# Kernel optimization log

Measured on AMD Instinct MI355X. Metric: run time of the kernel, lower is better.

The kernel has to match this reference:

```python
import jax, jax.numpy as jnp
import numpy as np

# Static config (matches init_kwargs)
DIM, HEADS = 192, 6
PL, LAT, LON = 8, 96, 180
WP, WL, WW = 2, 6, 12          # window size (pressure, lat, lon)
SP, SL, SW = 1, 3, 6           # shift size
N = WP * WL * WW               # tokens per window = 144
NPL, NLAT, NLON = PL // WP, LAT // WL, LON // WW   # 4, 16, 15
NW = NPL * NLAT                # type_of_windows = 64 (lat/pl-dependent bias)
HD = DIM // HEADS              # 32
L = PL * LAT * LON
BIAS_LEN = (2 * WW - 1) * WL * WL * WP * WP   # 3312
EPS = 1e-5


def _position_index():
    # Earth-specific relative position index (Pangu): absolute-position
    # dependence along pressure and latitude, relative along longitude.
    zi = np.arange(WP); zj = -np.arange(WP) * WP
    hi = np.arange(WL); hj = -np.arange(WL) * WL
    w = np.arange(WW)
    c1 = np.stack(np.meshgrid(zi, hi, w, indexing='ij')).reshape(3, -1)
    c2 = np.stack(np.meshgrid(zj, hj, w, indexing='ij')).reshape(3, -1)
    c = (c1[:, :, None] - c2[:, None, :]).transpose(1, 2, 0).copy()
    c[:, :, 2] += WW - 1
    c[:, :, 1] *= 2 * WW - 1
    c[:, :, 0] *= (2 * WW - 1) * WL * WL
    return c.sum(-1)  # (N, N) in [0, BIAS_LEN)


def _attn_mask():
    # Shifted-window mask: lon is periodic on the globe (roll only), so
    # masking is applied along pressure and latitude boundaries only.
    img = np.zeros((1, PL, LAT, LON, 1), np.float32)
    cnt = 0
    for pl in (slice(0, -WP), slice(-WP, -SP), slice(-SP, None)):
        for la in (slice(0, -WL), slice(-WL, -SL), slice(-SL, None)):
            img[:, pl, la, :, :] = cnt
            cnt += 1
    mw = img.reshape(1, NPL, WP, NLAT, WL, NLON, WW, 1)
    mw = mw.transpose(0, 5, 1, 3, 2, 4, 6, 7).reshape(NLON, NW, N)
    am = mw[:, :, None, :] - mw[:, :, :, None]
    return np.where(am != 0, -100.0, 0.0).astype(np.float32)  # (NLON, NW, N, N)


POS_IDX = jnp.asarray(_position_index())
ATTN_MASK = jnp.asarray(_attn_mask())


def layer_norm(x, g, b):
    m = x.mean(-1, keepdims=True)
    v = ((x - m) ** 2).mean(-1, keepdims=True)
    return (x - m) * jax.lax.rsqrt(v + EPS) * g + b


def setup_inputs() -> dict:
    key = jax.random.key(0)
    ks = jax.random.split(key, 10)
    s = 0.02
    return {
        'x': jax.random.normal(ks[0], (1, L, DIM), jnp.float32),
        'norm1_g': jnp.ones((DIM,), jnp.float32),
        'norm1_b': jnp.zeros((DIM,), jnp.float32),
        'qkv_w': jax.random.normal(ks[1], (DIM, 3 * DIM), jnp.float32) * s,
        'qkv_b': jnp.zeros((3 * DIM,), jnp.float32),
        'earth_bias': jax.random.normal(ks[2], (BIAS_LEN, NW, HEADS), jnp.float32) * s,
        'proj_w': jax.random.normal(ks[3], (DIM, DIM), jnp.float32) * s,
        'proj_b': jnp.zeros((DIM,), jnp.float32),
        'norm2_g': jnp.ones((DIM,), jnp.float32),
        'norm2_b': jnp.zeros((DIM,), jnp.float32),
        'fc1_w': jax.random.normal(ks[4], (DIM, 4 * DIM), jnp.float32) * s,
        'fc1_b': jnp.zeros((4 * DIM,), jnp.float32),
        'fc2_w': jax.random.normal(ks[5], (4 * DIM, DIM), jnp.float32) * s,
        'fc2_b': jnp.zeros((DIM,), jnp.float32),
    }


def reference(x, norm1_g, norm1_b, qkv_w, qkv_b, earth_bias, proj_w, proj_b,
              norm2_g, norm2_b, fc1_w, fc1_b, fc2_w, fc2_b):
    B, Ltok, C = x.shape
    shortcut = x
    h = layer_norm(x, norm1_g, norm1_b).reshape(B, PL, LAT, LON, C)
    # shifted windows (lon is periodic -> plain roll)
    h = jnp.roll(h, shift=(-SP, -SL, -SW), axis=(1, 2, 3))
    # window partition -> (B*NLON, NW, N, C); lon windows folded into batch
    xw = h.reshape(B, NPL, WP, NLAT, WL, NLON, WW, C)
    xw = xw.transpose(0, 5, 1, 3, 2, 4, 6, 7).reshape(B * NLON, NW, N, C)
    # earth-specific attention
    qkv = (xw @ qkv_w + qkv_b).reshape(B * NLON, NW, N, 3, HEADS, HD)
    qkv = qkv.transpose(3, 0, 1, 4, 2, 5)  # (3, B_, NW, H, N, HD)
    q, k, v = qkv[0], qkv[1], qkv[2]
    attn = jnp.einsum('bwhnd,bwhmd->bwhnm', q * (HD ** -0.5), k)
    bias = earth_bias[POS_IDX].reshape(N, N, NW, HEADS).transpose(2, 3, 0, 1)
    attn = attn + bias[None]                        # (B_, NW, H, N, N)
    attn = attn.reshape(B, NLON, NW, HEADS, N, N) + ATTN_MASK[None, :, :, None]
    attn = jax.nn.softmax(attn.reshape(B * NLON, NW, HEADS, N, N), axis=-1)
    out = jnp.einsum('bwhnm,bwhmd->bwhnd', attn, v)
    out = out.transpose(0, 1, 3, 2, 4).reshape(B * NLON, NW, N, C)
    out = out @ proj_w + proj_b
    # window reverse + roll back
    h = out.reshape(B, NLON, NPL, NLAT, WP, WL, WW, C)
    h = h.transpose(0, 2, 4, 3, 5, 1, 6, 7).reshape(B, PL, LAT, LON, C)
    h = jnp.roll(h, shift=(SP, SL, SW), axis=(1, 2, 3)).reshape(B, Ltok, C)
    x = shortcut + h
    # MLP block (GELU exact, as nn.GELU default)
    y = layer_norm(x, norm2_g, norm2_b)
    y = jax.nn.gelu(y @ fc1_w + fc1_b, approximate=False) @ fc2_w + fc2_b
    return x + y
```

## Files before the change

### kernel.cpp

```cpp
#include <hip/hip_runtime.h>
#include <hip/hip_bf16.h>
#include <math.h>

typedef unsigned short u16;
typedef __attribute__((ext_vector_type(8))) short short8;
typedef __attribute__((ext_vector_type(4))) short short4v;
typedef __attribute__((ext_vector_type(4))) float f32x4;

#define MFMA(a,b,c) __builtin_amdgcn_mfma_f32_16x16x32_bf16(a,b,c,0,0,0)
#define DIM 192

__device__ __forceinline__ float bf2f(u16 u){ unsigned v=((unsigned)u)<<16; float f; __builtin_memcpy(&f,&v,4); return f; }
__device__ __forceinline__ u16 f2bf(float f){ unsigned v; __builtin_memcpy(&v,&f,4); v = v + 0x7fffu + ((v>>16)&1u); return (u16)(v>>16); }

__device__ __forceinline__ void gl_lds16(const u16* g, u16* l){
  __builtin_amdgcn_global_load_lds((const __attribute__((address_space(1))) unsigned int*)g,
                                   (__attribute__((address_space(3))) unsigned int*)l, 16, 0, 0);
}

__device__ __forceinline__ int win_to_tok(int r){
  int lon = r/9216; int rem = r - lon*9216;
  int w = rem/144, n = rem - w*144;
  int ip=w>>4, il=w&15;
  int wp=n/72, t=n-wp*72, wl=t/12, ww=t-wl*12;
  int p=ip*2+wp, la=il*6+wl, lo=lon*12+ww;
  int p0=p+1;  if(p0>=8)   p0-=8;
  int la0=la+3; if(la0>=96) la0-=96;
  int lo0=lo+6; if(lo0>=180)lo0-=180;
  return (p0*96+la0)*180+lo0;
}

__global__ __launch_bounds__(256) void ln1_window_kernel(
    const float* __restrict__ x, const float* __restrict__ g, const float* __restrict__ b,
    u16* __restrict__ A)
{
  int r = blockIdx.x*4 + (threadIdx.x>>6);
  int lane = threadIdx.x & 63;
  size_t src = (size_t)win_to_tok(r)*DIM;
  float v0=x[src+lane], v1=x[src+64+lane], v2=x[src+128+lane];
  float s=v0+v1+v2;
  for(int m=32;m>=1;m>>=1) s += __shfl_xor(s,m);
  float mean = s*(1.f/192.f);
  float d0=v0-mean,d1=v1-mean,d2=v2-mean;
  float q=d0*d0+d1*d1+d2*d2;
  for(int m=32;m>=1;m>>=1) q += __shfl_xor(q,m);
  float rstd = rsqrtf(q*(1.f/192.f)+1e-5f);
  size_t o = (size_t)r*DIM;
  A[o+lane]     = f2bf(d0*rstd*g[lane]     + b[lane]);
  A[o+64+lane]  = f2bf(d1*rstd*g[64+lane]  + b[64+lane]);
  A[o+128+lane] = f2bf(d2*rstd*g[128+lane] + b[128+lane]);
}

__global__ __launch_bounds__(256) void transpose_bf16_kernel(
    const float* __restrict__ src, u16* __restrict__ dst, int K, int N)
{
  int idx = blockIdx.x*256 + threadIdx.x;
  if (idx >= K*N) return;
  int k = idx / N, n = idx - k*N;
  dst[n*K + k] = f2bf(src[idx]);
}

__global__ __launch_bounds__(256) void pf_w1_kernel(const float* __restrict__ fc1w, u16* __restrict__ W1f){
  int idx = blockIdx.x*256 + threadIdx.x;
  int e = idx & 7, g3 = idx >> 3;
  int g = g3 % 24, r3 = g3 / 24;
  int r = r3 & 31, hc = r3 >> 5;
  int k = ((g ^ (r&7))<<3) + e;
  W1f[idx] = f2bf(fc1w[(size_t)k*768 + hc*32 + r]);
}
__global__ __launch_bounds__(256) void pf_w2_kernel(const float* __restrict__ fc2w, u16* __restrict__ W2f){
  int idx = blockIdx.x*256 + threadIdx.x;
  int e = idx & 7, g3 = idx >> 3;
  int g = g3 & 3, r3 = g3 >> 2;
  int r = r3 % 192, hc = r3 / 192;
  int k = hc*32 + ((g ^ (r&3))<<3) + e;
  W2f[idx] = f2bf(fc2w[(size_t)k*192 + r]);
}

__global__ __launch_bounds__(256) void bias_expand_kernel(
    const float* __restrict__ eb, u16* __restrict__ B2)
{
  __shared__ int t1s[144], t2s[144], rgs[144];
  __shared__ float ebs[3312];
  int bid = blockIdx.x;
  int w = bid / 6;
  int tid = threadIdx.x;
  if (tid < 144) {
    int n = tid;
    int wp=n/72, t=n-wp*72, wl=t/12, ww=t-wl*12;
    t1s[n] = wp*828 + wl*23 + ww;
    t2s[n] = 1656*wp + 138*wl - ww + 11;
    int ip = w>>4, il = w&15;
    int p = ip*2+wp, la = il*6+wl;
    int rp = (p<6)?0:((p<7)?1:2);
    int rl = (la<90)?0:((la<93)?1:2);
    rgs[n] = rp*3+rl;
  }
  for (int i = tid; i < 3312; i += 256) ebs[i] = eb[(size_t)i*384 + bid];
  __syncthreads();
  size_t ob = (size_t)bid*20736;
  for (int idx = tid; idx < 20736; idx += 256) {
    int i = idx & 3, lane = (idx>>2)&63, t = idx>>8;
    int mt = t%9, nt = t/9;
    int n = nt*16 + (lane&15);
    int m = mt*16 + ((lane>>4)<<2) + i;
    float bv = ebs[t1s[n]+t2s[m]];
    bv += (rgs[n]==rgs[m]) ? 0.f : -100.f;
    B2[ob + idx] = f2bf(bv);
  }
}

#define SM_WS   0
#define SM_QS   38400
#define SM_KS   49920
#define SM_VS   61440
#define SM_PS   72192
#define SMEM3   120576

__global__ __launch_bounds__(576) void attn_kernel(
    const u16* __restrict__ A,
    const u16* __restrict__ Wt,
    const float* __restrict__ qkvb,
    const u16* __restrict__ Bexp,
    u16* __restrict__ O)
{
  extern __shared__ char smem[];
  u16* Ws = (u16*)(smem + SM_WS);
  u16* qs = (u16*)(smem + SM_QS);
  u16* ks_= (u16*)(smem + SM_KS);
  u16* vs = (u16*)(smem + SM_VS);
  u16* Ps = (u16*)(smem + SM_PS);

  int bid = blockIdx.x;
  int logical = (bid & 7)*720 + (bid >> 3);
  int lon = logical % 15;
  int wh  = logical / 15;
  int h = wh % 6, w = wh / 6;
  int tid = threadIdx.x, lane = tid & 63, wv = tid >> 6;

  {
    int rr = tid % 96, chunk = tid / 96;
    int mat = rr >> 5, c = rr & 31;
    const u16* s = Wt + (size_t)(mat*192 + h*32 + c)*192 + chunk*32;
    u16* d = Ws + rr*200 + chunk*32;
    *(uint4*)(d)    = *(const uint4*)(s);
    *(uint4*)(d+8)  = *(const uint4*)(s+8);
    *(uint4*)(d+16) = *(const uint4*)(s+16);
    *(uint4*)(d+24) = *(const uint4*)(s+24);
  }
  if (tid < 512) { int c = tid>>4; vs[c*168 + 144 + (tid&15)] = 0; }
  for (int j=0;j<4;j++){ int idx = tid + j*576; int row = idx>>4;
    if (row < 144) Ps[row*168 + 144 + (idx&15)] = 0; }
  __syncthreads();

  size_t winbase = (size_t)(lon*64 + w)*144;
  int r0 = wv*16;
  int l15 = lane & 15, lg = lane >> 4;

  short8 af[6];
  {
    const u16* arow = A + (winbase + r0 + l15)*DIM + 8*lg;
    #pragma unroll
    for (int k0=0;k0<6;k0++) af[k0] = *(const short8*)(arow + k0*32);
  }
  const float qscale = 0.17677669529663687f;

  #pragma unroll
  for (int mt=0; mt<2; mt++) {
    f32x4 acc = {0.f,0.f,0.f,0.f};
    const u16* wrow = Ws + (mt*16 + l15)*200 + 8*lg;
    #pragma unroll
    for (int k0=0;k0<6;k0++) acc = MFMA(*(const short8*)(wrow + k0*32), af[k0], acc);
    short4v pk;
    #pragma unroll
    for (int i=0;i<4;i++) pk[i] = (short)f2bf((acc[i] + qkvb[h*32 + mt*16 + 4*lg + i])*qscale);
    *(short4v*)(qs + (r0 + l15)*40 + mt*16 + 4*lg) = pk;
  }
  #pragma unroll
  for (int mt=0; mt<2; mt++) {
    f32x4 acc = {0.f,0.f,0.f,0.f};
    const u16* wrow = Ws + (32 + mt*16 + l15)*200 + 8*lg;
    #pragma unroll
    for (int k0=0;k0<6;k0++) acc = MFMA(*(const short8*)(wrow + k0*32), af[k0], acc);
    short4v pk;
    #pragma unroll
    for (int i=0;i<4;i++) pk[i] = (short)f2bf(acc[i] + qkvb[192 + h*32 + mt*16 + 4*lg + i]);
    *(short4v*)(ks_ + (r0 + l15)*40 + mt*16 + 4*lg) = pk;
  }
  #pragma unroll
  for (int ct=0; ct<2; ct++) {
    f32x4 acc = {0.f,0.f,0.f,0.f};
    const u16* wrow = Ws + (64 + ct*16 + l15)*200 + 8*lg;
    #pragma unroll
    for (int k0=0;k0<6;k0++) acc = MFMA(af[k0], *(const short8*)(wrow + k0*32), acc);
    float bias = qkvb[384 + h*32 + ct*16 + l15];
    short4v pk;
    #pragma unroll
    for (int i=0;i<4;i++) pk[i] = (short)f2bf(acc[i] + bias);
    *(short4v*)(vs + (ct*16 + l15)*168 + r0 + 4*lg) = pk;
  }
  __syncthreads();

  short8 bq = *(const short8*)(qs + (r0 + l15)*40 + 8*lg);
  f32x4 sa[9];
  #pragma unroll
  for (int mt=0; mt<9; mt++) {
    f32x4 z = {0.f,0.f,0.f,0.f};
    sa[mt] = MFMA(*(const short8*)(ks_ + (mt*16 + l15)*40 + 8*lg), bq, z);
  }
  {
    const u16* bb = Bexp + (((size_t)wh*9 + wv)*9)*256 + lane*4;
    #pragma unroll
    for (int mt=0; mt<9; mt++) {
      short4v pk = *(const short4v*)(bb + mt*256);
      #pragma unroll
      for (int i=0;i<4;i++) sa[mt][i] += bf2f((u16)pk[i]);
    }
  }
  float rsum = 0.f;
  #pragma unroll
  for (int mt=0; mt<9; mt++)
    #pragma unroll
    for (int i=0;i<4;i++) { float e = __expf(sa[mt][i]); sa[mt][i] = e; rsum += e; }
  rsum += __shfl_xor(rsum, 16);
  rsum += __shfl_xor(rsum, 32);
  float rinv = 1.f / rsum;
  #pragma unroll
  for (int mt=0; mt<9; mt++) {
    short4v pk;
    #pragma unroll
    for (int i=0;i<4;i++) pk[i] = (short)f2bf(sa[mt][i]);
    *(short4v*)(Ps + (r0 + l15)*168 + mt*16 + 4*lg) = pk;
  }

  #pragma unroll
  for (int ct2=0; ct2<2; ct2++) {
    f32x4 acc = {0.f,0.f,0.f,0.f};
    const u16* vr = vs + (ct2*16 + l15)*168 + 8*lg;
    const u16* pr = Ps + (r0 + l15)*168 + 8*lg;
    #pragma unroll
    for (int k0=0;k0<5;k0++) acc = MFMA(*(const short8*)(vr + 32*k0), *(const short8*)(pr + 32*k0), acc);
    short4v pk;
    #pragma unroll
    for (int i=0;i<4;i++) pk[i] = (short)f2bf(acc[i]*rinv);
    *(short4v*)(O + (winbase + r0 + l15)*DIM + h*32 + ct2*16 + 4*lg) = pk;
  }
}

#define SMEMP (73728 + 512)
__global__ __launch_bounds__(512, 4) void proj_ln2_kernel(
    const u16* __restrict__ AT,
    const u16* __restrict__ Pw,
    const float* __restrict__ pb, const float* __restrict__ x,
    const float* __restrict__ n2g, const float* __restrict__ n2b,
    float* __restrict__ out, u16* __restrict__ Y)
{
  extern __shared__ char smem[];
  u16* Pws = (u16*)smem;
  int* tokmap = (int*)(smem + 73728);
  int tid = threadIdx.x;
  size_t rbase = (size_t)blockIdx.x*128;
  #pragma unroll
  for (int j=0;j<9;j++){
    int g = j*512 + tid;
    int row = g/24, jj = g - row*24;
    uint4 t = *(const uint4*)(Pw + (size_t)row*192 + jj*8);
    *(uint4*)(Pws + row*192 + ((jj ^ (row&7))*8)) = t;
  }
  if (tid < 128) tokmap[tid] = win_to_tok((int)rbase + tid);
  __syncthreads();

  int lane = tid&63, wv = tid>>6, r0 = wv*16;
  int l15 = lane&15, lg = lane>>4;
  short8 af[6];
  const u16* arow = AT + (rbase + r0 + l15)*DIM + 8*lg;
  #pragma unroll
  for (int k0=0;k0<6;k0++) af[k0] = *(const short8*)(arow + k0*32);

  f32x4 acc[12];
  #pragma unroll
  for (int ct=0; ct<12; ct++) {
    f32x4 a = {0.f,0.f,0.f,0.f};
    const u16* wr = Pws + (ct*16+l15)*192;
    #pragma unroll
    for (int k0=0;k0<6;k0++) a = MFMA(af[k0], *(const short8*)(wr + (((k0*4+lg)^(l15&7))*8)), a);
    acc[ct] = a;
  }
  int toks[4];
  #pragma unroll
  for (int i=0;i<4;i++) toks[i] = tokmap[r0 + 4*lg + i];
  #pragma unroll
  for (int ct=0; ct<12; ct++) {
    int col = ct*16+l15;
    float bias = pb[col];
    #pragma unroll
    for (int i=0;i<4;i++){
      size_t o = (size_t)toks[i]*DIM + col;
      float v = x[o] + acc[ct][i] + bias;
      out[o] = v;
      acc[ct][i] = v;
    }
  }
  float s[4] = {0,0,0,0};
  #pragma unroll
  for (int ct=0; ct<12; ct++) for (int i=0;i<4;i++) s[i] += acc[ct][i];
  #pragma unroll
  for (int i=0;i<4;i++){ for (int m=1;m<16;m<<=1) s[i] += __shfl_xor(s[i], m, 16); s[i] *= (1.f/192.f); }
  float q[4] = {0,0,0,0};
  #pragma unroll
  for (int ct=0; ct<12; ct++) for (int i=0;i<4;i++){ float d = acc[ct][i]-s[i]; q[i] += d*d; }
  #pragma unroll
  for (int i=0;i<4;i++){ for (int m=1;m<16;m<<=1) q[i] += __shfl_xor(q[i], m, 16); q[i] = rsqrtf(q[i]*(1.f/192.f)+1e-5f); }
  #pragma unroll
  for (int ct=0; ct<12; ct++) {
    int col = ct*16+l15;
    float gg = n2g[col], bb = n2b[col];
    #pragma unroll
    for (int i=0;i<4;i++)
      Y[(size_t)toks[i]*DIM + col] = f2bf((acc[ct][i]-s[i])*q[i]*gg + bb);
  }
}

#define SMEM5 59392
__global__ __launch_bounds__(512, 4) void mlp_kernel(
    const u16* __restrict__ Y,
    const u16* __restrict__ W1f,
    const float* __restrict__ b1,
    const u16* __restrict__ W2f,
    const float* __restrict__ b2,
    float* __restrict__ out)
{
  extern __shared__ char smem[];
  u16* W1b0 = (u16*)smem;
  u16* W1b1 = (u16*)(smem + 12288);
  u16* W2b0 = (u16*)(smem + 24576);
  u16* W2b1 = (u16*)(smem + 36864);
  u16* Hs   = (u16*)(smem + 49152);
  int tid = threadIdx.x;
  size_t rbase = (size_t)blockIdx.x*128;
  int lane = tid&63, wv = tid>>6, r0 = wv*16;
  int l15 = lane&15, lg = lane>>4;

  short8 af[6];
  {
    const u16* yrow = Y + (rbase + r0 + l15)*DIM + 8*lg;
    #pragma unroll
    for (int k0=0;k0<6;k0++) af[k0] = *(const short8*)(yrow + k0*32);
  }

  {
    gl_lds16(W1f + (size_t)tid*8, W1b0 + tid*8);
    if (tid < 256) gl_lds16(W1f + (size_t)(512+tid)*8, W1b0 + (512+tid)*8);
    gl_lds16(W2f + (size_t)tid*8, W2b0 + tid*8);
    if (tid < 256) gl_lds16(W2f + (size_t)(512+tid)*8, W2b0 + (512+tid)*8);
    const u16* s1 = W1f + 6144; const u16* s2 = W2f + 6144;
    gl_lds16(s1 + (size_t)tid*8, W1b1 + tid*8);
    if (tid < 256) gl_lds16(s1 + (size_t)(512+tid)*8, W1b1 + (512+tid)*8);
    gl_lds16(s2 + (size_t)tid*8, W2b1 + tid*8);
    if (tid < 256) gl_lds16(s2 + (size_t)(512+tid)*8, W2b1 + (512+tid)*8);
  }
  __syncthreads();

  f32x4 acc2[12];
  #pragma unroll
  for (int i=0;i<12;i++) acc2[i] = (f32x4){0.f,0.f,0.f,0.f};

  const float GA = -1.5957691216057307f;
  const float GB = -0.07135481627272283f;

  for (int hc=0; hc<24; hc++) {
    u16* B1w = (hc&1) ? W1b1 : W1b0;
    u16* B2w = (hc&1) ? W2b1 : W2b0;
    #pragma unroll
    for (int ct=0; ct<2; ct++) {
      f32x4 a1 = {0.f,0.f,0.f,0.f};
      const u16* wr = B1w + (ct*16+l15)*192;
      #pragma unroll
      for (int k0=0;k0<6;k0++) a1 = MFMA(af[k0], *(const short8*)(wr + (((k0*4+lg)^(l15&7))*8)), a1);
      float bb = b1[hc*32 + ct*16 + l15];
      #pragma unroll
      for (int i=0;i<4;i++){
        float v = a1[i] + bb;
        float t = v*v;
        float m = fmaf(t, GB, GA);
        float e = __expf(v*m);
        float hgl = v*__builtin_amdgcn_rcpf(1.f + e);
        Hs[(r0 + 4*lg + i)*40 + ct*16 + l15] = f2bf(hgl);
      }
    }
    {
      short8 ah = *(const short8*)(Hs + (r0+l15)*40 + 8*lg);
      #pragma unroll
      for (int ct2=0; ct2<12; ct2++) {
        const u16* wr2 = B2w + (ct2*16+l15)*32 + ((lg ^ (l15&3))*8);
        acc2[ct2] = MFMA(ah, *(const short8*)(wr2), acc2[ct2]);
      }
    }
    __syncthreads();
    if (hc < 22) {
      const u16* s1 = W1f + (size_t)(hc+2)*6144;
      const u16* s2 = W2f + (size_t)(hc+2)*6144;
      u16* d1 = (hc&1) ? W1b1 : W1b0;
      u16* d2 = (hc&1) ? W2b1 : W2b0;
      gl_lds16(s1 + (size_t)tid*8, d1 + tid*8);
      if (tid < 256) gl_lds16(s1 + (size_t)(512+tid)*8, d1 + (512+tid)*8);
      gl_lds16(s2 + (size_t)tid*8, d2 + tid*8);
      if (tid < 256) gl_lds16(s2 + (size_t)(512+tid)*8, d2 + (512+tid)*8);
    }
  }
  #pragma unroll
  for (int ct2=0; ct2<12; ct2++) {
    int col = ct2*16+l15;
    float bb = b2[col];
    #pragma unroll
    for (int i=0;i<4;i++){
      size_t o = (rbase + r0 + 4*lg + i)*DIM + col;
      out[o] = out[o] + acc2[ct2][i] + bb;
    }
  }
}

extern "C" void kernel_launch(void* const* d_in, const int* in_sizes, int n_in,
                              void* d_out, int out_size, void* d_ws, size_t ws_size,
                              hipStream_t stream) {
  const float* x    = (const float*)d_in[0];
  const float* n1g  = (const float*)d_in[1];
  const float* n1b  = (const float*)d_in[2];
  const float* qkvw = (const float*)d_in[3];
  const float* qkvb = (const float*)d_in[4];
  const float* eb   = (const float*)d_in[5];
  const float* projw= (const float*)d_in[6];
  const float* projb= (const float*)d_in[7];
  const float* n2g  = (const float*)d_in[8];
  const float* n2b  = (const float*)d_in[9];
  const float* fc1w = (const float*)d_in[10];
  const float* fc1b = (const float*)d_in[11];
  const float* fc2w = (const float*)d_in[12];
  const float* fc2b = (const float*)d_in[13];
  float* out = (float*)d_out;
  char* ws = (char*)d_ws;

  u16* A   = (u16*)(ws);
  u16* AT  = (u16*)(ws + 53084160);
  u16* Wq  = (u16*)(ws + 106168320);
  u16* Pw  = (u16*)(ws + 106389504);
  u16* W1f = (u16*)(ws + 106463232);
  u16* W2f = (u16*)(ws + 106758144);
  u16* Bexp = (u16*)d_out;

  hipFuncSetAttribute((const void*)attn_kernel,     hipFuncAttributeMaxDynamicSharedMemorySize, SMEM3);
  hipFuncSetAttribute((const void*)proj_ln2_kernel, hipFuncAttributeMaxDynamicSharedMemorySize, SMEMP);
  hipFuncSetAttribute((const void*)mlp_kernel,      hipFuncAttributeMaxDynamicSharedMemorySize, SMEM5);

  transpose_bf16_kernel<<<432, 256, 0, stream>>>(qkvw, Wq, 192, 576);
  transpose_bf16_kernel<<<144, 256, 0, stream>>>(projw, Pw, 192, 192);
  pf_w1_kernel<<<576, 256, 0, stream>>>(fc1w, W1f);
  pf_w2_kernel<<<576, 256, 0, stream>>>(fc2w, W2f);
  bias_expand_kernel<<<384, 256, 0, stream>>>(eb, Bexp);
  ln1_window_kernel<<<34560, 256, 0, stream>>>(x, n1g, n1b, A);
  attn_kernel<<<5760, 576, SMEM3, stream>>>(A, Wq, qkvb, Bexp, AT);
  proj_ln2_kernel<<<1080, 512, SMEMP, stream>>>(AT, Pw, projb, x, n2g, n2b, out, A);
  mlp_kernel<<<1080, 512, SMEM5, stream>>>(A, W1f, fc1b, W2f, fc2b, out);
}
```

Before: 469.0 us.

## Alias P buffer onto weight smem and XOR-swizzle weight tile to shrink LDS

The attention kernel's LDS is cut from about 118KB to about 69KB. The weight tile drops its row padding and uses an XOR swizzle on 16-byte groups to avoid bank conflicts, and the softmax probability buffer now reuses the weight region after an added barrier. The smaller LDS footprint should let two 576-thread blocks share a CU, raising occupancy. The cost is one extra block-wide synchronisation and per-row zeroing of the P padding.

```diff
diff --git a/kernel.cpp b/kernel.cpp
--- a/kernel.cpp
+++ b/kernel.cpp
@@ -111,11 +111,11 @@
 }
 
 #define SM_WS   0
-#define SM_QS   38400
-#define SM_KS   49920
-#define SM_VS   61440
-#define SM_PS   72192
-#define SMEM3   120576
+#define SM_QS   36864
+#define SM_KS   48384
+#define SM_VS   59904
+#define SM_PS   0
+#define SMEM3   70656
 
 __global__ __launch_bounds__(576) void attn_kernel(
     const u16* __restrict__ A,
@@ -142,20 +142,24 @@
     int rr = tid % 96, chunk = tid / 96;
     int mat = rr >> 5, c = rr & 31;
     const u16* s = Wt + (size_t)(mat*192 + h*32 + c)*192 + chunk*32;
-    u16* d = Ws + rr*200 + chunk*32;
-    *(uint4*)(d)    = *(const uint4*)(s);
-    *(uint4*)(d+8)  = *(const uint4*)(s+8);
-    *(uint4*)(d+16) = *(const uint4*)(s+16);
-    *(uint4*)(d+24) = *(const uint4*)(s+24);
+    uint4 t0 = *(const uint4*)(s);
+    uint4 t1 = *(const uint4*)(s+8);
+    uint4 t2 = *(const uint4*)(s+16);
+    uint4 t3 = *(const uint4*)(s+24);
+    u16* d = Ws + rr*192;
+    int r7 = rr & 7, g0 = chunk*4;
+    *(uint4*)(d + ((g0  )^r7)*8) = t0;
+    *(uint4*)(d + ((g0+1)^r7)*8) = t1;
+    *(uint4*)(d + ((g0+2)^r7)*8) = t2;
+    *(uint4*)(d + ((g0+3)^r7)*8) = t3;
   }
   if (tid < 512) { int c = tid>>4; vs[c*168 + 144 + (tid&15)] = 0; }
-  for (int j=0;j<4;j++){ int idx = tid + j*576; int row = idx>>4;
-    if (row < 144) Ps[row*168 + 144 + (idx&15)] = 0; }
   __syncthreads();
 
   size_t winbase = (size_t)(lon*64 + w)*144;
   int r0 = wv*16;
   int l15 = lane & 15, lg = lane >> 4;
+  int sw7 = l15 & 7;
 
   short8 af[6];
   {
@@ -168,9 +172,9 @@
   #pragma unroll
   for (int mt=0; mt<2; mt++) {
     f32x4 acc = {0.f,0.f,0.f,0.f};
-    const u16* wrow = Ws + (mt*16 + l15)*200 + 8*lg;
-    #pragma unroll
-    for (int k0=0;k0<6;k0++) acc = MFMA(*(const short8*)(wrow + k0*32), af[k0], acc);
+    const u16* wrow = Ws + (mt*16 + l15)*192;
+    #pragma unroll
+    for (int k0=0;k0<6;k0++) acc = MFMA(*(const short8*)(wrow + ((k0*4+lg)^sw7)*8), af[k0], acc);
     short4v pk;
     #pragma unroll
     for (int i=0;i<4;i++) pk[i] = (short)f2bf((acc[i] + qkvb[h*32 + mt*16 + 4*lg + i])*qscale);
@@ -179,9 +183,9 @@
   #pragma unroll
   for (int mt=0; mt<2; mt++) {
     f32x4 acc = {0.f,0.f,0.f,0.f};
-    const u16* wrow = Ws + (32 + mt*16 + l15)*200 + 8*lg;
-    #pragma unroll
-    for (int k0=0;k0<6;k0++) acc = MFMA(*(const short8*)(wrow + k0*32), af[k0], acc);
+    const u16* wrow = Ws + (32 + mt*16 + l15)*192;
+    #pragma unroll
+    for (int k0=0;k0<6;k0++) acc = MFMA(*(const short8*)(wrow + ((k0*4+lg)^sw7)*8), af[k0], acc);
     short4v pk;
     #pragma unroll
     for (int i=0;i<4;i++) pk[i] = (short)f2bf(acc[i] + qkvb[192 + h*32 + mt*16 + 4*lg + i]);
@@ -190,9 +194,9 @@
   #pragma unroll
   for (int ct=0; ct<2; ct++) {
     f32x4 acc = {0.f,0.f,0.f,0.f};
-    const u16* wrow = Ws + (64 + ct*16 + l15)*200 + 8*lg;
-    #pragma unroll
-    for (int k0=0;k0<6;k0++) acc = MFMA(af[k0], *(const short8*)(wrow + k0*32), acc);
+    const u16* wrow = Ws + (64 + ct*16 + l15)*192;
+    #pragma unroll
+    for (int k0=0;k0<6;k0++) acc = MFMA(af[k0], *(const short8*)(wrow + ((k0*4+lg)^sw7)*8), acc);
     float bias = qkvb[384 + h*32 + ct*16 + l15];
     short4v pk;
     #pragma unroll
@@ -208,6 +212,8 @@
     f32x4 z = {0.f,0.f,0.f,0.f};
     sa[mt] = MFMA(*(const short8*)(ks_ + (mt*16 + l15)*40 + 8*lg), bq, z);
   }
+  __syncthreads();
+
   {
     const u16* bb = Bexp + (((size_t)wh*9 + wv)*9)*256 + lane*4;
     #pragma unroll
@@ -231,6 +237,10 @@
     #pragma unroll
     for (int i=0;i<4;i++) pk[i] = (short)f2bf(sa[mt][i]);
     *(short4v*)(Ps + (r0 + l15)*168 + mt*16 + 4*lg) = pk;
+  }
+  {
+    short4v z = {0,0,0,0};
+    *(short4v*)(Ps + (r0 + l15)*168 + 144 + 4*lg) = z;
   }
 
   #pragma unroll
```

New measurement: 442.3 us. -5.7%, faster.
